# Kernel tuning notes

Measured on AMD Instinct MI355X. Metric: run time of the kernel, lower is better.

## Reference

```python
import jax, jax.numpy as jnp
import numpy as np

ROT = 256  # Hadamard block size (ConvLinear4bit._n)


def _hadamard(n):
    # Sylvester construction of the n x n Hadamard matrix (n power of 2)
    H = np.array([[1.0]], dtype=np.float32)
    while H.shape[0] < n:
        H = np.block([[H, H], [H, -H]])
    return jnp.asarray(H / np.sqrt(n), dtype=jnp.float32)


def setup_inputs() -> dict:
    key = jax.random.key(0)
    k1, k2, k3, k4 = jax.random.split(key, 4)
    N, D_in, D_out = 4096, 4096, 4096
    x = jax.random.normal(k1, (N, D_in), dtype=jnp.float32)
    # unpacked int4 weights in [-7, 7] (logical content of the packed uint8 buffer)
    weight_int = jax.random.randint(k2, (D_out, D_in), -7, 8, dtype=jnp.int32)
    # per-output-row weight scales (quarot: max|W_rot| / 7)
    w_scale = jax.random.uniform(k3, (D_out, 1), dtype=jnp.float32) * 0.01 + 1e-4
    bias = jax.random.normal(k4, (D_out,), dtype=jnp.float32) * 0.01
    return {"x": x, "weight_int": weight_int, "w_scale": w_scale, "bias": bias}


def reference(x, weight_int, w_scale, bias):
    N, D = x.shape
    H = _hadamard(ROT)
    # blockwise Hadamard rotation along the feature dim (D is a multiple of ROT)
    x_rot = (x.reshape(N, D // ROT, ROT) @ H).reshape(N, D)
    # per-row symmetric int4 quantization of activations
    scales_x = jnp.max(jnp.abs(x_rot), axis=-1, keepdims=True) / 7.0  # [N, 1]
    q_x = jnp.clip(jnp.round(x_rot / scales_x), -8, 7).astype(jnp.int32)
    acc = jnp.matmul(q_x, weight_int.T)
    # sym_dequant: row scale (activations) * col scale (weights), then bias
    out = acc.astype(jnp.float32) * scales_x * w_scale.T + bias
    return out
```

## Files before the change

kernel.cpp:

```cpp
#include <hip/hip_runtime.h>
#include <math.h>

typedef int v4i __attribute__((ext_vector_type(4)));

#define DIM 4096
#define BT 128
#define KT 64

__device__ __forceinline__ void async16(const void* g, void* l) {
    __builtin_amdgcn_global_load_lds((__attribute__((address_space(1))) void*)(g),
                                     (__attribute__((address_space(3))) void*)(l),
                                     16, 0, 0);
}

__global__ __launch_bounds__(256) void wconv(const int* __restrict__ w,
                                             signed char* __restrict__ w8) {
    int i = blockIdx.x * 256 + threadIdx.x;
    int4 v = ((const int4*)w)[i];
    char4 c;
    c.x = (signed char)v.x; c.y = (signed char)v.y;
    c.z = (signed char)v.z; c.w = (signed char)v.w;
    ((char4*)w8)[i] = c;
}

__global__ __launch_bounds__(256) void rotquant(const float* __restrict__ x,
                                                signed char* __restrict__ q,
                                                float* __restrict__ scales) {
    const int row  = blockIdx.x;
    const int lane = threadIdx.x & 63;
    const int wave = threadIdx.x >> 6;
    const float* xr = x + (size_t)row * DIM;

    float f[4][4];
    #pragma unroll
    for (int b = 0; b < 4; ++b) {
        const int base = (wave + 4 * b) * 256;
        #pragma unroll
        for (int j = 0; j < 4; ++j) f[b][j] = xr[base + j * 64 + lane];
        #pragma unroll
        for (int d = 1; d <= 32; d <<= 1) {
            #pragma unroll
            for (int j = 0; j < 4; ++j) {
                float p = __shfl_xor(f[b][j], d, 64);
                f[b][j] = (lane & d) ? (p - f[b][j]) : (f[b][j] + p);
            }
        }
        float t0 = f[b][0] + f[b][1], t1 = f[b][0] - f[b][1];
        float t2 = f[b][2] + f[b][3], t3 = f[b][2] - f[b][3];
        f[b][0] = (t0 + t2) * 0.0625f;
        f[b][1] = (t1 + t3) * 0.0625f;
        f[b][2] = (t0 - t2) * 0.0625f;
        f[b][3] = (t1 - t3) * 0.0625f;
    }

    float m = 0.0f;
    #pragma unroll
    for (int b = 0; b < 4; ++b)
        #pragma unroll
        for (int j = 0; j < 4; ++j) m = fmaxf(m, fabsf(f[b][j]));
    #pragma unroll
    for (int d = 32; d; d >>= 1) m = fmaxf(m, __shfl_xor(m, d, 64));
    __shared__ float sm[4];
    if (lane == 0) sm[wave] = m;
    __syncthreads();
    m = fmaxf(fmaxf(sm[0], sm[1]), fmaxf(sm[2], sm[3]));

    const float s = m / 7.0f;
    if (threadIdx.x == 0) scales[row] = s;

    signed char* qr = q + (size_t)row * DIM;
    #pragma unroll
    for (int b = 0; b < 4; ++b) {
        const int base = (wave + 4 * b) * 256;
        #pragma unroll
        for (int j = 0; j < 4; ++j) {
            int qi = (int)rintf(f[b][j] / s);
            qi = min(7, max(-8, qi));
            qr[base + j * 64 + lane] = (signed char)qi;
        }
    }
}

__global__ __launch_bounds__(256) void gemm_q8(const signed char* __restrict__ A,
                                               const signed char* __restrict__ B,
                                               const float* __restrict__ rowScale,
                                               const float* __restrict__ wscale,
                                               const float* __restrict__ bias,
                                               float* __restrict__ out) {
    __shared__ __align__(16) signed char As[BT * KT];
    __shared__ __align__(16) signed char Bs[BT * KT];

    const int bm = blockIdx.y, bn = blockIdx.x;
    const int t = threadIdx.x;
    const int lane = t & 63, wave = t >> 6;
    const int wm = (wave >> 1) * 64, wn = (wave & 1) * 64;
    const int quad = lane >> 4, mr = lane & 15;

    v4i acc[4][4] = {};

    for (int kt = 0; kt < DIM; kt += KT) {
        __syncthreads();
        #pragma unroll
        for (int h = 0; h < 2; ++h) {
            const int cidx = t + 256 * h;
            const int row  = cidx >> 2;
            const int sw   = (cidx & 3) ^ (row & 3);
            async16(A + (size_t)(bm * BT + row) * DIM + kt + sw * 16, &As[cidx * 16]);
            async16(B + (size_t)(bn * BT + row) * DIM + kt + sw * 16, &Bs[cidx * 16]);
        }
        __syncthreads();

        v4i a[4], b[4];
        #pragma unroll
        for (int i = 0; i < 4; ++i) {
            const int r = wm + i * 16 + mr;
            a[i] = *(const v4i*)&As[r * KT + ((quad ^ (r & 3)) * 16)];
            const int c = wn + i * 16 + mr;
            b[i] = *(const v4i*)&Bs[c * KT + ((quad ^ (c & 3)) * 16)];
        }
        #pragma unroll
        for (int i = 0; i < 4; ++i)
            #pragma unroll
            for (int j = 0; j < 4; ++j)
                acc[i][j] = __builtin_amdgcn_mfma_i32_16x16x64_i8(a[i], b[j], acc[i][j], 0, 0, 0);
    }

    #pragma unroll
    for (int j = 0; j < 4; ++j) {
        const int col = bn * BT + wn + j * 16 + mr;
        const float ws = wscale[col];
        const float bs = bias[col];
        #pragma unroll
        for (int i = 0; i < 4; ++i) {
            #pragma unroll
            for (int r = 0; r < 4; ++r) {
                const int row = bm * BT + wm + i * 16 + quad * 4 + r;
                out[(size_t)row * DIM + col] =
                    ((float)acc[i][j][r] * rowScale[row]) * ws + bs;
            }
        }
    }
}

extern "C" void kernel_launch(void* const* d_in, const int* in_sizes, int n_in,
                              void* d_out, int out_size, void* d_ws, size_t ws_size,
                              hipStream_t stream) {
    const float* x      = (const float*)d_in[0];
    const int*   wint   = (const int*)d_in[1];
    const float* wscale = (const float*)d_in[2];
    const float* bias   = (const float*)d_in[3];
    float* out = (float*)d_out;

    signed char* q8 = (signed char*)d_ws;
    signed char* w8 = q8 + (size_t)DIM * DIM;
    float* sx = (float*)(w8 + (size_t)DIM * DIM);

    wconv<<<(DIM * DIM / 4) / 256, 256, 0, stream>>>(wint, w8);
    rotquant<<<DIM, 256, 0, stream>>>(x, q8, sx);
    gemm_q8<<<dim3(DIM / BT, DIM / BT), 256, 0, stream>>>(q8, w8, sx, wscale, bias, out);
}
```

Measured before the change: 264.3 us.

## Double GEMM K-tile with 8-way swizzle and vectorize rotquant loads/stores

The GEMM K tile grows from 64 to 128 bytes. This halves the number of barrier-separated load/compute iterations, and the LDS XOR swizzle is widened from 4 to 8 groups to match. The Hadamard rotation kernel now reads float4 per lane, does the in-register radix-4 butterfly first, replaces the branchy shuffle butterfly with an fmaf by a precomputed sign, and writes char4 per lane. The larger tile doubles LDS use per block (32KB), which may reduce occupancy, and loads are still not overlapped with compute.

```diff
diff --git a/kernel.cpp b/kernel.cpp
--- a/kernel.cpp
+++ b/kernel.cpp
@@ -5,7 +5,7 @@
 
 #define DIM 4096
 #define BT 128
-#define KT 64
+#define KT 128
 
 __device__ __forceinline__ void async16(const void* g, void* l) {
     __builtin_amdgcn_global_load_lds((__attribute__((address_space(1))) void*)(g),
@@ -29,28 +29,32 @@
     const int row  = blockIdx.x;
     const int lane = threadIdx.x & 63;
     const int wave = threadIdx.x >> 6;
-    const float* xr = x + (size_t)row * DIM;
+    const float4* xr4 = (const float4*)(x + (size_t)row * DIM);
+
+    float sgn[6];
+    #pragma unroll
+    for (int i = 0; i < 6; ++i) sgn[i] = (lane & (1 << i)) ? -1.0f : 1.0f;
 
     float f[4][4];
     #pragma unroll
     for (int b = 0; b < 4; ++b) {
-        const int base = (wave + 4 * b) * 256;
+        const int blk = wave + 4 * b;
+        float4 v = xr4[blk * 64 + lane];
+        float t0 = v.x + v.y, t1 = v.x - v.y;
+        float t2 = v.z + v.w, t3 = v.z - v.w;
+        f[b][0] = t0 + t2; f[b][1] = t1 + t3;
+        f[b][2] = t0 - t2; f[b][3] = t1 - t3;
         #pragma unroll
-        for (int j = 0; j < 4; ++j) f[b][j] = xr[base + j * 64 + lane];
-        #pragma unroll
-        for (int d = 1; d <= 32; d <<= 1) {
+        for (int st = 0; st < 6; ++st) {
+            const int m = 1 << st;
             #pragma unroll
             for (int j = 0; j < 4; ++j) {
-                float p = __shfl_xor(f[b][j], d, 64);
-                f[b][j] = (lane & d) ? (p - f[b][j]) : (f[b][j] + p);
+                float p = __shfl_xor(f[b][j], m, 64);
+                f[b][j] = fmaf(sgn[st], f[b][j], p);
             }
         }
-        float t0 = f[b][0] + f[b][1], t1 = f[b][0] - f[b][1];
-        float t2 = f[b][2] + f[b][3], t3 = f[b][2] - f[b][3];
-        f[b][0] = (t0 + t2) * 0.0625f;
-        f[b][1] = (t1 + t3) * 0.0625f;
-        f[b][2] = (t0 - t2) * 0.0625f;
-        f[b][3] = (t1 - t3) * 0.0625f;
+        #pragma unroll
+        for (int j = 0; j < 4; ++j) f[b][j] *= 0.0625f;
     }
 
     float m = 0.0f;
@@ -68,16 +72,17 @@
     const float s = m / 7.0f;
     if (threadIdx.x == 0) scales[row] = s;
 
-    signed char* qr = q + (size_t)row * DIM;
+    char4* qr4 = (char4*)(q + (size_t)row * DIM);
     #pragma unroll
     for (int b = 0; b < 4; ++b) {
-        const int base = (wave + 4 * b) * 256;
-        #pragma unroll
-        for (int j = 0; j < 4; ++j) {
-            int qi = (int)rintf(f[b][j] / s);
-            qi = min(7, max(-8, qi));
-            qr[base + j * 64 + lane] = (signed char)qi;
-        }
+        const int blk = wave + 4 * b;
+        char4 c;
+        int qi;
+        qi = (int)rintf(f[b][0] / s); c.x = (signed char)min(7, max(-8, qi));
+        qi = (int)rintf(f[b][1] / s); c.y = (signed char)min(7, max(-8, qi));
+        qi = (int)rintf(f[b][2] / s); c.z = (signed char)min(7, max(-8, qi));
+        qi = (int)rintf(f[b][3] / s); c.w = (signed char)min(7, max(-8, qi));
+        qr4[blk * 64 + lane] = c;
     }
 }
 
@@ -101,28 +106,32 @@
     for (int kt = 0; kt < DIM; kt += KT) {
         __syncthreads();
         #pragma unroll
-        for (int h = 0; h < 2; ++h) {
+        for (int h = 0; h < 4; ++h) {
             const int cidx = t + 256 * h;
-            const int row  = cidx >> 2;
-            const int sw   = (cidx & 3) ^ (row & 3);
-            async16(A + (size_t)(bm * BT + row) * DIM + kt + sw * 16, &As[cidx * 16]);
-            async16(B + (size_t)(bn * BT + row) * DIM + kt + sw * 16, &Bs[cidx * 16]);
+            const int row  = cidx >> 3;
+            const int g    = (cidx & 7) ^ (row & 7);
+            async16(A + (size_t)(bm * BT + row) * DIM + kt + g * 16, &As[cidx * 16]);
+            async16(B + (size_t)(bn * BT + row) * DIM + kt + g * 16, &Bs[cidx * 16]);
         }
         __syncthreads();
 
-        v4i a[4], b[4];
         #pragma unroll
-        for (int i = 0; i < 4; ++i) {
-            const int r = wm + i * 16 + mr;
-            a[i] = *(const v4i*)&As[r * KT + ((quad ^ (r & 3)) * 16)];
-            const int c = wn + i * 16 + mr;
-            b[i] = *(const v4i*)&Bs[c * KT + ((quad ^ (c & 3)) * 16)];
+        for (int s = 0; s < 2; ++s) {
+            v4i a[4], b[4];
+            #pragma unroll
+            for (int i = 0; i < 4; ++i) {
+                const int r = wm + i * 16 + mr;
+                const int c = wn + i * 16 + mr;
+                const int cl = s * 4 + quad;
+                a[i] = *(const v4i*)&As[r * KT + ((cl ^ (r & 7)) * 16)];
+                b[i] = *(const v4i*)&Bs[c * KT + ((cl ^ (c & 7)) * 16)];
+            }
+            #pragma unroll
+            for (int i = 0; i < 4; ++i)
+                #pragma unroll
+                for (int j = 0; j < 4; ++j)
+                    acc[i][j] = __builtin_amdgcn_mfma_i32_16x16x64_i8(a[i], b[j], acc[i][j], 0, 0, 0);
         }
-        #pragma unroll
-        for (int i = 0; i < 4; ++i)
-            #pragma unroll
-            for (int j = 0; j < 4; ++j)
-                acc[i][j] = __builtin_amdgcn_mfma_i32_16x16x64_i8(a[i], b[j], acc[i][j], 0, 0, 0);
     }
 
     #pragma unroll
```

Result: faster. 253.4 us (-4.1%).
